# Performance work log

Measured on AMD Instinct MI355X. Metric: run time of the kernel, lower is better.

The kernel has to match this reference:

```python
import jax, jax.numpy as jnp
import numpy as np

NUM_HEADS = 8  # attention_head_size = C // NUM_HEADS, used only for score scaling


def conv1x1(x, w, b):
    # x: [B, Cin, H, W], w: [Cout, Cin], b: [Cout]
    return jnp.einsum('bchw,oc->bohw', x, w) + b[None, :, None, None]


def setup_inputs() -> dict:
    key = jax.random.key(0)
    ks = jax.random.split(key, 10)
    B, C, H, W = 8, 256, 96, 96
    x = jax.random.normal(ks[0], (B, C, H, W), dtype=jnp.float32)
    y = jax.random.normal(ks[1], (B, 1, 24, 24), dtype=jnp.float32)
    s = 0.02
    wy = jax.random.normal(ks[2], (C, 1), dtype=jnp.float32) * s
    by = jnp.zeros((C,), dtype=jnp.float32)
    wq = jax.random.normal(ks[3], (C, C), dtype=jnp.float32) * s
    bq = jnp.zeros((C,), dtype=jnp.float32)
    wk = jax.random.normal(ks[4], (C, C), dtype=jnp.float32) * s
    bk = jnp.zeros((C,), dtype=jnp.float32)
    wv = jax.random.normal(ks[5], (C, C), dtype=jnp.float32) * s
    bv = jnp.zeros((C,), dtype=jnp.float32)
    return {'x': x, 'y': y, 'wy': wy, 'by': by, 'wq': wq, 'bq': bq,
            'wk': wk, 'bk': bk, 'wv': wv, 'bv': bv}


def reference(x, y, wy, by, wq, bq, wk, bk, wv, bv):
    B, C, H, W = x.shape
    head_size = C // NUM_HEADS
    # x branch
    xq = conv1x1(x, wq, bq)
    xk = conv1x1(x, wk, bk)
    v = conv1x1(x, wv, bv)
    # y branch: 1 -> C channels, bilinear upsample (align_corners=False == half-pixel)
    y2 = conv1x1(y, wy, by)
    y2 = jax.image.resize(y2, (B, C, H, W), method='bilinear')
    yq = conv1x1(y2, wq, bq)
    yk = conv1x1(y2, wk, bk)
    # gated Q/K
    q = (xq * yq).transpose(0, 2, 1, 3)  # [B, H, C, W]
    k = (xk * yk).transpose(0, 2, 1, 3)
    vt = v.transpose(0, 2, 1, 3)
    # channel attention per spatial row: scores [B, H, C, C]
    scores = jnp.einsum('bhcw,bhdw->bhcd', q, k) / jnp.sqrt(jnp.asarray(head_size, x.dtype))
    probs = jax.nn.softmax(scores, axis=-1)
    out = jnp.einsum('bhcd,bhdw->bhcw', probs, vt)
    return out.transpose(0, 2, 1, 3)  # [B, C, H, W]
```

## Files before the change

kernel.cpp:

```cpp
#include <hip/hip_runtime.h>

typedef __bf16 bf16;
typedef __attribute__((ext_vector_type(8))) __bf16 bf16x8;
typedef __attribute__((ext_vector_type(4))) __bf16 bf16x4;
typedef __attribute__((ext_vector_type(4))) float f32x4;

#define MFMA16(A, B, C) __builtin_amdgcn_mfma_f32_16x16x32_bf16(A, B, C, 0, 0, 0)

static __device__ __forceinline__ void wave_lgkm_wait() {
  asm volatile("s_waitcnt lgkmcnt(0)" ::: "memory");
}

__global__ __launch_bounds__(256) void k_prep(
    const float* __restrict__ y, const float* __restrict__ wy, const float* __restrict__ by,
    const float* __restrict__ wq, const float* __restrict__ bq,
    const float* __restrict__ wk, const float* __restrict__ bk,
    const float* __restrict__ wv,
    bf16* __restrict__ wq_bf, bf16* __restrict__ wk_bf, bf16* __restrict__ wv_bf,
    float* __restrict__ yu, float* __restrict__ aq, float* __restrict__ cq,
    float* __restrict__ ak, float* __restrict__ ck)
{
  int blk = blockIdx.x, t = threadIdx.x;
  if (blk < 192) {
    int idx4 = blk * 256 + t;
    int fo = idx4 * 4;
    const float* src; bf16* dst; int off;
    if (fo < 65536)       { src = wq; dst = wq_bf; off = fo; }
    else if (fo < 131072) { src = wk; dst = wk_bf; off = fo - 65536; }
    else                  { src = wv; dst = wv_bf; off = fo - 131072; }
    float4 v = *(const float4*)(src + off);
    bf16x4 o;
    o[0] = (bf16)v.x; o[1] = (bf16)v.y; o[2] = (bf16)v.z; o[3] = (bf16)v.w;
    *(bf16x4*)(dst + off) = o;
  } else if (blk < 200) {
    int b = blk - 192;
    const float* yb = y + b * 576;
#pragma unroll 1
    for (int i = 0; i < 36; ++i) {
      int e = t + i * 256;
      int oh = e / 96, ow = e % 96;
      float sh = oh * 0.25f - 0.375f;
      float sw = ow * 0.25f - 0.375f;
      int ih0 = (int)floorf(sh);
      int iw0 = (int)floorf(sw);
      float fh = sh - (float)ih0, fw = sw - (float)iw0;
      int ih0c = min(23, max(0, ih0)), ih1c = min(23, max(0, ih0 + 1));
      int iw0c = min(23, max(0, iw0)), iw1c = min(23, max(0, iw0 + 1));
      float v00 = yb[ih0c * 24 + iw0c], v01 = yb[ih0c * 24 + iw1c];
      float v10 = yb[ih1c * 24 + iw0c], v11 = yb[ih1c * 24 + iw1c];
      yu[b * 9216 + e] = (1.0f - fh) * ((1.0f - fw) * v00 + fw * v01)
                       + fh * ((1.0f - fw) * v10 + fw * v11);
    }
  } else {
    int ol = t >> 5, cl = t & 31;
    int o = (blk - 200) * 8 + ol;
    int c0 = cl * 8;
    float4 wy0 = *(const float4*)(wy + c0), wy1 = *(const float4*)(wy + c0 + 4);
    float4 by0 = *(const float4*)(by + c0), by1 = *(const float4*)(by + c0 + 4);
    float4 q0  = *(const float4*)(wq + o * 256 + c0), q1 = *(const float4*)(wq + o * 256 + c0 + 4);
    float4 k0  = *(const float4*)(wk + o * 256 + c0), k1 = *(const float4*)(wk + o * 256 + c0 + 4);
    float wyv[8] = {wy0.x, wy0.y, wy0.z, wy0.w, wy1.x, wy1.y, wy1.z, wy1.w};
    float byv[8] = {by0.x, by0.y, by0.z, by0.w, by1.x, by1.y, by1.z, by1.w};
    float qv[8]  = {q0.x, q0.y, q0.z, q0.w, q1.x, q1.y, q1.z, q1.w};
    float kv[8]  = {k0.x, k0.y, k0.z, k0.w, k1.x, k1.y, k1.z, k1.w};
    float saq = 0.f, scq = 0.f, sak = 0.f, sck = 0.f;
#pragma unroll
    for (int j = 0; j < 8; ++j) {
      saq += qv[j] * wyv[j]; scq += qv[j] * byv[j];
      sak += kv[j] * wyv[j]; sck += kv[j] * byv[j];
    }
#pragma unroll
    for (int s = 16; s >= 1; s >>= 1) {
      saq += __shfl_xor(saq, s, 32);
      scq += __shfl_xor(scq, s, 32);
      sak += __shfl_xor(sak, s, 32);
      sck += __shfl_xor(sck, s, 32);
    }
    if (cl == 0) {
      aq[o] = saq; cq[o] = scq + bq[o];
      ak[o] = sak; ck[o] = sck + bk[o];
    }
  }
}

__global__ __launch_bounds__(1024, 1) void k_fused(
    const float* __restrict__ x, const float* __restrict__ yu,
    const bf16* __restrict__ wq_bf, const bf16* __restrict__ wk_bf, const bf16* __restrict__ wv_bf,
    const float* __restrict__ bq, const float* __restrict__ bk, const float* __restrict__ bv,
    const float* __restrict__ aq, const float* __restrict__ cq,
    const float* __restrict__ ak, const float* __restrict__ ck,
    float* __restrict__ out)
{
  __shared__ __align__(16) bf16 xs[96 * 264];
  __shared__ __align__(16) bf16 ks[256 * 104];

  int pl = blockIdx.x;
  int b = pl / 96, h = pl % 96;
  int t = threadIdx.x;
  int wid = t >> 6, lane = t & 63;
  int l15 = lane & 15, g = lane >> 4;
  int otile = wid * 16;

  {
    const float* xrow = x + (size_t)b * 2359296 + (size_t)h * 96;
#pragma unroll
    for (int i = 0; i < 3; ++i) {
      int tsk = i * 1024 + t;
      int w = tsk % 96;
      int c0 = (tsk / 96) * 8;
      float v[8];
#pragma unroll
      for (int j = 0; j < 8; ++j) v[j] = xrow[(size_t)(c0 + j) * 9216 + w];
      bf16x8 o8;
#pragma unroll
      for (int j = 0; j < 8; ++j) o8[j] = (bf16)v[j];
      *(bf16x8*)(xs + w * 264 + c0) = o8;
    }
  }
  __syncthreads();

  const float SC = 0.17677669529663687f;
  bf16* stg = ks + otile * 104;

  bf16x8 qf[3];

  {
    f32x4 qacc[6] = {};
    f32x4 kacc[6] = {};
    f32x4 vacc[6] = {};
#pragma unroll 1
    for (int kq = 0; kq < 8; ++kq) {
      const bf16* xp = xs + kq * 32 + g * 8;
      bf16x8 A[6];
#pragma unroll
      for (int m = 0; m < 6; ++m)
        A[m] = *(const bf16x8*)(xp + (m * 16 + l15) * 264);
      size_t wo = (size_t)(otile + l15) * 256 + kq * 32 + g * 8;
      bf16x8 Bq = *(const bf16x8*)(wq_bf + wo);
      bf16x8 Bk = *(const bf16x8*)(wk_bf + wo);
      bf16x8 Bv = *(const bf16x8*)(wv_bf + wo);
#pragma unroll
      for (int m = 0; m < 6; ++m) {
        qacc[m] = MFMA16(A[m], Bq, qacc[m]);
        kacc[m] = MFMA16(A[m], Bk, kacc[m]);
        vacc[m] = MFMA16(Bv, A[m], vacc[m]);
      }
    }

    float4 yv[6];
    {
      const float* yr = yu + (size_t)pl * 96;
#pragma unroll
      for (int mt = 0; mt < 6; ++mt)
        yv[mt] = *(const float4*)(yr + mt * 16 + g * 4);
    }
    int o = otile + l15;
    float bqv = bq[o], aq0 = aq[o], cq0 = cq[o];
    float bkv = bk[o], ak0 = ak[o], ck0 = ck[o];

#pragma unroll
    for (int m = 0; m < 6; ++m) {
      float yy[4] = {yv[m].x, yv[m].y, yv[m].z, yv[m].w};
      bf16x4 pk;
#pragma unroll
      for (int r = 0; r < 4; ++r)
        pk[r] = (bf16)((qacc[m][r] + bqv) * (yy[r] * aq0 + cq0) * SC);
      *(bf16x4*)(stg + l15 * 104 + m * 16 + g * 4) = pk;
    }
    wave_lgkm_wait();
#pragma unroll
    for (int kk = 0; kk < 3; ++kk)
      qf[kk] = *(const bf16x8*)(stg + l15 * 104 + kk * 32 + g * 8);
    wave_lgkm_wait();

#pragma unroll
    for (int m = 0; m < 6; ++m) {
      float yy[4] = {yv[m].x, yv[m].y, yv[m].z, yv[m].w};
      bf16x4 pk;
#pragma unroll
      for (int r = 0; r < 4; ++r)
        pk[r] = (bf16)((kacc[m][r] + bkv) * (yy[r] * ak0 + ck0));
      *(bf16x4*)(ks + (size_t)o * 104 + m * 16 + g * 4) = pk;
    }

    float4 bm = *(const float4*)(bv + otile + g * 4);
    float bb[4] = {bm.x, bm.y, bm.z, bm.w};
    __syncthreads();
    bf16* vs = xs;
    int vbase = (otile & ~16) + ((otile >> 2) & 4);
#pragma unroll
    for (int n = 0; n < 6; ++n) {
      bf16x4 pk;
#pragma unroll
      for (int r = 0; r < 4; ++r) pk[r] = (bf16)(vacc[n][r] + bb[r]);
      *(bf16x4*)(vs + (size_t)(n * 16 + l15) * 264 + vbase + g * 8) = pk;
    }
  }
  __syncthreads();

  const bf16* vs = xs;
  f32x4 oacc[6] = {};
  float lp = 0.f;

  bf16x8 KA[6], KB[6];
  {
    const bf16* kp = ks + (size_t)l15 * 104 + g * 8;
#pragma unroll
    for (int kk = 0; kk < 3; ++kk)
#pragma unroll
      for (int dn = 0; dn < 2; ++dn)
        KA[kk * 2 + dn] = *(const bf16x8*)(kp + (size_t)(dn * 16) * 104 + kk * 32);
  }

  auto attn_step = [&](int dt, bf16x8* Kc, bf16x8* Kn, bool pf) {
    int d0 = dt * 32;
    if (pf) {
      const bf16* kp = ks + (size_t)((dt + 1) * 32 + l15) * 104 + g * 8;
#pragma unroll
      for (int kk = 0; kk < 3; ++kk)
#pragma unroll
        for (int dn = 0; dn < 2; ++dn)
          Kn[kk * 2 + dn] = *(const bf16x8*)(kp + (size_t)(dn * 16) * 104 + kk * 32);
    }
    f32x4 s0 = {}, s1 = {};
    __builtin_amdgcn_s_setprio(1);
#pragma unroll
    for (int kk = 0; kk < 3; ++kk) {
      s0 = MFMA16(Kc[kk * 2 + 0], qf[kk], s0);
      s1 = MFMA16(Kc[kk * 2 + 1], qf[kk], s1);
    }
    __builtin_amdgcn_s_setprio(0);
    bf16x8 pa;
#pragma unroll
    for (int r = 0; r < 4; ++r) {
      float e0 = __expf(s0[r]);
      float e1 = __expf(s1[r]);
      lp += e0 + e1;
      pa[r] = (bf16)e0;
      pa[4 + r] = (bf16)e1;
    }
    const bf16* vp = vs + (size_t)l15 * 264 + d0 + g * 8;
    __builtin_amdgcn_s_setprio(1);
#pragma unroll
    for (int n = 0; n < 6; ++n) {
      bf16x8 Bv = *(const bf16x8*)(vp + (size_t)n * 16 * 264);
      oacc[n] = MFMA16(pa, Bv, oacc[n]);
    }
    __builtin_amdgcn_s_setprio(0);
  };

#pragma unroll 1
  for (int dt2 = 0; dt2 < 4; ++dt2) {
    attn_step(2 * dt2,     KA, KB, true);
    attn_step(2 * dt2 + 1, KB, KA, 2 * dt2 + 1 < 7);
  }

  float vsum = lp;
  vsum += __shfl_xor(vsum, 16, 64);
  vsum += __shfl_xor(vsum, 32, 64);
  float inv = 1.0f / vsum;
  float invr[4];
#pragma unroll
  for (int r = 0; r < 4; ++r)
    invr[r] = __shfl(inv, g * 4 + r, 16);

  __syncthreads();
  float* fst = (float*)ks;
  int s_hi = wid >> 3;
  int lr = (wid & 7) * 16;
  float* ob = out + (size_t)b * 2359296 + (size_t)h * 96;
#pragma unroll 1
  for (int s = 0; s < 2; ++s) {
    if (s_hi == s) {
#pragma unroll
      for (int n = 0; n < 6; ++n)
#pragma unroll
        for (int r = 0; r < 4; ++r)
          fst[(lr + g * 4 + r) * 100 + n * 16 + l15] = oacc[n][r] * invr[r];
    }
    __syncthreads();
    int ob0 = s * 128;
#pragma unroll
    for (int it = 0; it < 3; ++it) {
      int idx = it * 1024 + t;
      int row = idx / 24, col = idx - row * 24;
      float4 v4 = *(const float4*)(fst + row * 100 + col * 4);
      *(float4*)(ob + (size_t)(ob0 + row) * 9216 + col * 4) = v4;
    }
    __syncthreads();
  }
}

extern "C" void kernel_launch(void* const* d_in, const int* in_sizes, int n_in,
                              void* d_out, int out_size, void* d_ws, size_t ws_size,
                              hipStream_t stream) {
  const float* x  = (const float*)d_in[0];
  const float* y  = (const float*)d_in[1];
  const float* wy = (const float*)d_in[2];
  const float* by = (const float*)d_in[3];
  const float* wq = (const float*)d_in[4];
  const float* bq = (const float*)d_in[5];
  const float* wk = (const float*)d_in[6];
  const float* bk = (const float*)d_in[7];
  const float* wv = (const float*)d_in[8];
  const float* bv = (const float*)d_in[9];
  float* out = (float*)d_out;

  char* wsb = (char*)d_ws;
  bf16* wq_bf = (bf16*)(wsb);
  bf16* wk_bf = (bf16*)(wsb + 131072);
  bf16* wv_bf = (bf16*)(wsb + 262144);
  float* yu   = (float*)(wsb + 393216);
  float* aq   = (float*)(wsb + 688128);
  float* cq   = (float*)(wsb + 689152);
  float* ak   = (float*)(wsb + 690176);
  float* ck   = (float*)(wsb + 691200);

  hipLaunchKernelGGL(k_prep, dim3(232), dim3(256), 0, stream,
                     y, wy, by, wq, bq, wk, bk, wv,
                     wq_bf, wk_bf, wv_bf, yu, aq, cq, ak, ck);
  hipLaunchKernelGGL(k_fused, dim3(768), dim3(1024), 0, stream,
                     x, yu, wq_bf, wk_bf, wv_bf, bq, bk, bv,
                     aq, cq, ak, ck, out);
}
```

Baseline: 216.1 us.

## Prefetch weights, build Q fragments in registers, store output directly

The weight B-fragments are now software-pipelined one k-step ahead in the projection loop. Q operand fragments are assembled directly from accumulator registers, dropping the LDS staging round-trip and its waits. K fragments are read as two 4-wide halves with a permuted k order, and the final output skips the LDS transpose and its barriers, writing straight to global memory in scalar stores. The direct output stores coalesce less well, with 16 consecutive floats per row rather than float4 rows, and weight prefetch adds register pressure.

```diff
diff --git a/kernel.cpp b/kernel.cpp
--- a/kernel.cpp
+++ b/kernel.cpp
@@ -6,10 +6,6 @@
 typedef __attribute__((ext_vector_type(4))) float f32x4;
 
 #define MFMA16(A, B, C) __builtin_amdgcn_mfma_f32_16x16x32_bf16(A, B, C, 0, 0, 0)
-
-static __device__ __forceinline__ void wave_lgkm_wait() {
-  asm volatile("s_waitcnt lgkmcnt(0)" ::: "memory");
-}
 
 __global__ __launch_bounds__(256) void k_prep(
     const float* __restrict__ y, const float* __restrict__ wy, const float* __restrict__ by,
@@ -117,10 +113,15 @@
       *(bf16x8*)(xs + w * 264 + c0) = o8;
     }
   }
+
+  size_t wo0 = (size_t)(otile + l15) * 256 + g * 8;
+  bf16x8 Bq_c = *(const bf16x8*)(wq_bf + wo0);
+  bf16x8 Bk_c = *(const bf16x8*)(wk_bf + wo0);
+  bf16x8 Bv_c = *(const bf16x8*)(wv_bf + wo0);
+
   __syncthreads();
 
   const float SC = 0.17677669529663687f;
-  bf16* stg = ks + otile * 104;
 
   bf16x8 qf[3];
 
@@ -130,21 +131,25 @@
     f32x4 vacc[6] = {};
 #pragma unroll 1
     for (int kq = 0; kq < 8; ++kq) {
+      bf16x8 Bq_n, Bk_n, Bv_n;
+      if (kq < 7) {
+        size_t wo = wo0 + (kq + 1) * 32;
+        Bq_n = *(const bf16x8*)(wq_bf + wo);
+        Bk_n = *(const bf16x8*)(wk_bf + wo);
+        Bv_n = *(const bf16x8*)(wv_bf + wo);
+      }
       const bf16* xp = xs + kq * 32 + g * 8;
       bf16x8 A[6];
 #pragma unroll
       for (int m = 0; m < 6; ++m)
         A[m] = *(const bf16x8*)(xp + (m * 16 + l15) * 264);
-      size_t wo = (size_t)(otile + l15) * 256 + kq * 32 + g * 8;
-      bf16x8 Bq = *(const bf16x8*)(wq_bf + wo);
-      bf16x8 Bk = *(const bf16x8*)(wk_bf + wo);
-      bf16x8 Bv = *(const bf16x8*)(wv_bf + wo);
 #pragma unroll
       for (int m = 0; m < 6; ++m) {
-        qacc[m] = MFMA16(A[m], Bq, qacc[m]);
-        kacc[m] = MFMA16(A[m], Bk, kacc[m]);
-        vacc[m] = MFMA16(Bv, A[m], vacc[m]);
+        qacc[m] = MFMA16(A[m], Bq_c, qacc[m]);
+        kacc[m] = MFMA16(A[m], Bk_c, kacc[m]);
+        vacc[m] = MFMA16(Bv_c, A[m], vacc[m]);
       }
+      Bq_c = Bq_n; Bk_c = Bk_n; Bv_c = Bv_n;
     }
 
     float4 yv[6];
@@ -159,19 +164,18 @@
     float bkv = bk[o], ak0 = ak[o], ck0 = ck[o];
 
 #pragma unroll
-    for (int m = 0; m < 6; ++m) {
-      float yy[4] = {yv[m].x, yv[m].y, yv[m].z, yv[m].w};
-      bf16x4 pk;
-#pragma unroll
-      for (int r = 0; r < 4; ++r)
-        pk[r] = (bf16)((qacc[m][r] + bqv) * (yy[r] * aq0 + cq0) * SC);
-      *(bf16x4*)(stg + l15 * 104 + m * 16 + g * 4) = pk;
-    }
-    wave_lgkm_wait();
-#pragma unroll
-    for (int kk = 0; kk < 3; ++kk)
-      qf[kk] = *(const bf16x8*)(stg + l15 * 104 + kk * 32 + g * 8);
-    wave_lgkm_wait();
+    for (int kk = 0; kk < 3; ++kk) {
+      bf16x8 qq;
+#pragma unroll
+      for (int jh = 0; jh < 2; ++jh) {
+        int m = 2 * kk + jh;
+        float yy[4] = {yv[m].x, yv[m].y, yv[m].z, yv[m].w};
+#pragma unroll
+        for (int r = 0; r < 4; ++r)
+          qq[jh * 4 + r] = (bf16)((qacc[m][r] + bqv) * (yy[r] * aq0 + cq0) * SC);
+      }
+      qf[kk] = qq;
+    }
 
 #pragma unroll
     for (int m = 0; m < 6; ++m) {
@@ -202,26 +206,25 @@
   f32x4 oacc[6] = {};
   float lp = 0.f;
 
+  auto load_K = [&](int dt, bf16x8* K) {
+    const bf16* kp = ks + (size_t)(dt * 32 + l15) * 104 + g * 4;
+#pragma unroll
+    for (int kk = 0; kk < 3; ++kk)
+#pragma unroll
+      for (int dn = 0; dn < 2; ++dn) {
+        const bf16* p = kp + (size_t)(dn * 16) * 104 + kk * 32;
+        bf16x4 lo = *(const bf16x4*)(p);
+        bf16x4 hi = *(const bf16x4*)(p + 16);
+        K[kk * 2 + dn] = __builtin_shufflevector(lo, hi, 0, 1, 2, 3, 4, 5, 6, 7);
+      }
+  };
+
   bf16x8 KA[6], KB[6];
-  {
-    const bf16* kp = ks + (size_t)l15 * 104 + g * 8;
-#pragma unroll
-    for (int kk = 0; kk < 3; ++kk)
-#pragma unroll
-      for (int dn = 0; dn < 2; ++dn)
-        KA[kk * 2 + dn] = *(const bf16x8*)(kp + (size_t)(dn * 16) * 104 + kk * 32);
-  }
+  load_K(0, KA);
 
   auto attn_step = [&](int dt, bf16x8* Kc, bf16x8* Kn, bool pf) {
     int d0 = dt * 32;
-    if (pf) {
-      const bf16* kp = ks + (size_t)((dt + 1) * 32 + l15) * 104 + g * 8;
-#pragma unroll
-      for (int kk = 0; kk < 3; ++kk)
-#pragma unroll
-        for (int dn = 0; dn < 2; ++dn)
-          Kn[kk * 2 + dn] = *(const bf16x8*)(kp + (size_t)(dn * 16) * 104 + kk * 32);
-    }
+    if (pf) load_K(dt + 1, Kn);
     f32x4 s0 = {}, s1 = {};
     __builtin_amdgcn_s_setprio(1);
 #pragma unroll
@@ -264,30 +267,15 @@
   for (int r = 0; r < 4; ++r)
     invr[r] = __shfl(inv, g * 4 + r, 16);
 
-  __syncthreads();
-  float* fst = (float*)ks;
-  int s_hi = wid >> 3;
-  int lr = (wid & 7) * 16;
   float* ob = out + (size_t)b * 2359296 + (size_t)h * 96;
-#pragma unroll 1
-  for (int s = 0; s < 2; ++s) {
-    if (s_hi == s) {
-#pragma unroll
-      for (int n = 0; n < 6; ++n)
-#pragma unroll
-        for (int r = 0; r < 4; ++r)
-          fst[(lr + g * 4 + r) * 100 + n * 16 + l15] = oacc[n][r] * invr[r];
-    }
-    __syncthreads();
-    int ob0 = s * 128;
-#pragma unroll
-    for (int it = 0; it < 3; ++it) {
-      int idx = it * 1024 + t;
-      int row = idx / 24, col = idx - row * 24;
-      float4 v4 = *(const float4*)(fst + row * 100 + col * 4);
-      *(float4*)(ob + (size_t)(ob0 + row) * 9216 + col * 4) = v4;
-    }
-    __syncthreads();
+#pragma unroll
+  for (int n = 0; n < 6; ++n) {
+    int w = n * 16 + l15;
+#pragma unroll
+    for (int r = 0; r < 4; ++r) {
+      int o = otile + g * 4 + r;
+      ob[(size_t)o * 9216 + w] = oacc[n][r] * invr[r];
+    }
   }
 }
 
```

Result: no change. 216.2 us (+0.0%).
